# Kernel tuning notes

Hardware: AMD Instinct MI355X
Metric: run time of the kernel (lower is better)

Reference implementation:

```python
import jax, jax.numpy as jnp
import numpy as np


def setup_inputs() -> dict:
    key = jax.random.key(0)
    k1, k2, k3, k4 = jax.random.split(key, 4)
    b, s, h, z = 4, 4096, 2048, 64
    scale = 1.0 / np.sqrt(h)
    return {
        "hidden_states": jax.random.normal(k1, (b, s, h), dtype=jnp.float32),
        # nn.Linear(h, z, bias=False): store as (h, z) so y = x @ W
        "Wq": jax.random.normal(k2, (h, z), dtype=jnp.float32) * scale,
        "Wk": jax.random.normal(k3, (h, z), dtype=jnp.float32) * scale,
        "Wv": jax.random.normal(k4, (h, z), dtype=jnp.float32) * scale,
    }


def reference(hidden_states, Wq, Wk, Wv):
    b, s, h = hidden_states.shape
    z = Wq.shape[1]
    # Three small projections: (b, s, z), cast to float32 as in original
    q = jnp.einsum("bsh,hz->bsz", hidden_states, Wq).astype(jnp.float32)
    k = jnp.einsum("bsh,hz->bsz", hidden_states, Wk).astype(jnp.float32)
    v = jnp.einsum("bsh,hz->bsz", hidden_states, Wv).astype(jnp.float32)
    # Per-token outer product over the expert dim: (b, s, z, z)
    attn = q[..., :, None] * k[..., None, :]
    attn = jax.nn.softmax(attn, axis=-1)
    # Weighted sum over the key expert axis j: out[..., i] = sum_j attn[..., i, j] * v[..., j]
    out = jnp.einsum("bsij,bsj->bsi", attn, v)
    return out.reshape(b * s, z)
```

## Files before the change

kernel.cpp:

```cpp
#include <hip/hip_runtime.h>


typedef __bf16 bf16x8 __attribute__((ext_vector_type(8)));
typedef float f32x4  __attribute__((ext_vector_type(4)));

#define NTOK   16384
#define HDIM   2048
#define NCHUNK 64
#define KCH    32
#define CH_STRIDE (12 * 2 * 512)

#define SWZ(row, kq) ((kq) ^ ((row) & 7))

#define GLOAD_LDS16(g, l)                                                      \
  __builtin_amdgcn_global_load_lds(                                            \
      (const __attribute__((address_space(1))) void*)(g),                      \
      (__attribute__((address_space(3))) void*)(l), 16, 0, 0)

__global__ void pack_w_kernel(const float* __restrict__ Wq,
                              const float* __restrict__ Wk,
                              const float* __restrict__ Wv,
                              __bf16* __restrict__ bfrag)
{
  int u = blockIdx.x * blockDim.x + threadIdx.x;
  if (u >= NCHUNK * 12 * 64) return;
  int l  = u & 63;
  int tn = (u >> 6) % 12;
  int c  = u / (12 * 64);
  int n  = tn * 16 + (l & 15);
  int kb = c * 32 + ((l >> 4) << 3);
  const float* W = (n < 64) ? Wq : (n < 128) ? Wk : Wv;
  int nn = n & 63;
  bf16x8 hi, lo;
#pragma unroll
  for (int j = 0; j < 8; ++j) {
    float f = W[(size_t)(kb + j) * 64 + nn];
    __bf16 h = (__bf16)f;
    hi[j] = h;
    lo[j] = (__bf16)(f - (float)h);
  }
  size_t base = (size_t)(c * 12 + tn) * 1024 + (size_t)l * 8;
  *(bf16x8*)(bfrag + base)       = hi;
  *(bf16x8*)(bfrag + base + 512) = lo;
}

#define LOADB(S, cc)                                                           \
  {                                                                            \
    const __bf16* nbp = bp + (size_t)(cc) * CH_STRIDE;                         \
    _Pragma("unroll")                                                          \
    for (int t = 0; t < 3; ++t) {                                              \
      S##h[t] = *(const bf16x8*)(nbp + (size_t)t * 1024);                      \
      S##l[t] = *(const bf16x8*)(nbp + (size_t)t * 1024 + 512);                \
    }                                                                          \
  }

#define COMPUTE(ab, S)                                                         \
  {                                                                            \
    const int r0 = mr, r1 = 16 + mr;                                           \
    float4 A[4];                                                               \
    A[0] = *(const float4*)&(ab)[r0 * 32 + SWZ(r0, 2 * quad)     * 4];         \
    A[1] = *(const float4*)&(ab)[r0 * 32 + SWZ(r0, 2 * quad + 1) * 4];         \
    A[2] = *(const float4*)&(ab)[r1 * 32 + SWZ(r1, 2 * quad)     * 4];         \
    A[3] = *(const float4*)&(ab)[r1 * 32 + SWZ(r1, 2 * quad + 1) * 4];         \
    bf16x8 ah[2], al[2];                                                       \
    _Pragma("unroll")                                                          \
    for (int i = 0; i < 2; ++i) {                                              \
      float av[8] = {A[2*i].x, A[2*i].y, A[2*i].z, A[2*i].w,                   \
                     A[2*i+1].x, A[2*i+1].y, A[2*i+1].z, A[2*i+1].w};          \
      _Pragma("unroll")                                                        \
      for (int j = 0; j < 8; ++j) {                                            \
        __bf16 h = (__bf16)av[j];                                              \
        ah[i][j] = h;                                                          \
        al[i][j] = (__bf16)(av[j] - (float)h);                                 \
      }                                                                        \
    }                                                                          \
    _Pragma("unroll")                                                          \
    for (int i = 0; i < 2; ++i)                                                \
      _Pragma("unroll")                                                        \
      for (int t = 0; t < 3; ++t) {                                            \
        acc[i][t] = __builtin_amdgcn_mfma_f32_16x16x32_bf16(ah[i], S##h[t], acc[i][t], 0, 0, 0); \
        acc[i][t] = __builtin_amdgcn_mfma_f32_16x16x32_bf16(al[i], S##h[t], acc[i][t], 0, 0, 0); \
        acc[i][t] = __builtin_amdgcn_mfma_f32_16x16x32_bf16(ah[i], S##l[t], acc[i][t], 0, 0, 0); \
      }                                                                        \
  }

__global__ __launch_bounds__(512, 4) void router_kernel(
    const float* __restrict__ x,
    const __bf16* __restrict__ bfrag,
    float* __restrict__ out)
{
  const int tok0 = blockIdx.x * 32;
  const int w    = threadIdx.x >> 6;
  const int lane = threadIdx.x & 63;
  const int kh   = w >> 2;
  const int wc   = w & 3;
  const int mr   = lane & 15;
  const int quad = lane >> 4;

  __shared__ float qkv[2][32 * 196];
  __shared__ float bufA[2][2][1024];

  const int su   = threadIdx.x & 255;
  const int srow = su >> 3;
  const int skq  = su & 7;
  const float* aSrc = x + (size_t)(tok0 + srow) * HDIM + kh * 1024
                        + SWZ(srow, skq) * 4;
  float* aDst0 = &bufA[kh][0][(w & 3) * 256];
  float* aDst1 = &bufA[kh][1][(w & 3) * 256];

  const __bf16* bp = bfrag + (size_t)(kh * KCH) * CH_STRIDE
                           + (size_t)(3 * wc) * 1024 + (size_t)lane * 8;

  f32x4 acc[2][3];
#pragma unroll
  for (int i = 0; i < 2; ++i)
#pragma unroll
    for (int t = 0; t < 3; ++t)
      acc[i][t] = (f32x4){0.f, 0.f, 0.f, 0.f};

  bf16x8 B0h[3], B0l[3], B1h[3], B1l[3];

  GLOAD_LDS16(aSrc, aDst0);
  LOADB(B0, 0)
  __syncthreads();

  for (int c = 0; c < KCH; c += 2) {
    if (c + 1 < KCH) {
      GLOAD_LDS16(aSrc + (c + 1) * 32, aDst1);
      LOADB(B1, c + 1)
    }
    COMPUTE(bufA[kh][0], B0)
    __syncthreads();

    if (c + 2 < KCH) {
      GLOAD_LDS16(aSrc + (c + 2) * 32, aDst0);
      LOADB(B0, c + 2)
    }
    COMPUTE(bufA[kh][1], B1)
    __syncthreads();
  }

#pragma unroll
  for (int i = 0; i < 2; ++i)
#pragma unroll
    for (int t = 0; t < 3; ++t) {
      int col = wc * 48 + t * 16 + mr;
      int row = i * 16 + quad * 4;
#pragma unroll
      for (int r = 0; r < 4; ++r)
        qkv[kh][(row + r) * 196 + col] = acc[i][t][r];
    }
  __syncthreads();

  const int tt = threadIdx.x >> 4;
  const int g  = threadIdx.x & 15;
  const float* q0 = qkv[0] + tt * 196;
  const float* q1 = qkv[1] + tt * 196;
  float qs[4], lsum[4], osum[4];
#pragma unroll
  for (int ii = 0; ii < 4; ++ii) {
    qs[ii]   = (q0[g * 4 + ii] + q1[g * 4 + ii]) * 1.44269504f;
    lsum[ii] = 0.f;
    osum[ii] = 0.f;
  }
  for (int j = 0; j < 64; ++j) {
    float kj = q0[64 + j]  + q1[64 + j];
    float vj = q0[128 + j] + q1[128 + j];
#pragma unroll
    for (int ii = 0; ii < 4; ++ii) {
      float e = __builtin_amdgcn_exp2f(qs[ii] * kj);
      lsum[ii] += e;
      osum[ii] = fmaf(e, vj, osum[ii]);
    }
  }
  float4 r0v;
  r0v.x = osum[0] / lsum[0]; r0v.y = osum[1] / lsum[1];
  r0v.z = osum[2] / lsum[2]; r0v.w = osum[3] / lsum[3];
  float* op = out + (size_t)(tok0 + tt) * 64 + g * 4;
  *(float4*)op = r0v;
}

extern "C" void kernel_launch(void* const* d_in, const int* in_sizes, int n_in,
                              void* d_out, int out_size, void* d_ws, size_t ws_size,
                              hipStream_t stream)
{
  const float* x  = (const float*)d_in[0];
  const float* Wq = (const float*)d_in[1];
  const float* Wk = (const float*)d_in[2];
  const float* Wv = (const float*)d_in[3];
  __bf16* bfrag   = (__bf16*)d_ws;
  float*  out     = (float*)d_out;

  pack_w_kernel<<<(NCHUNK * 12 * 64 + 255) / 256, 256, 0, stream>>>(Wq, Wk, Wv, bfrag);
  router_kernel<<<NTOK / 32, 512, 0, stream>>>(x, bfrag, out);
}
```

Measured before the change: 240.8 us.

## Deepen global-load pipeline with inline-asm B loads and partial vmcnt waits

Replaces the compiler-generated B-fragment loads with inline-asm global_load_dwordx4 using immediate offsets. The main loop is restructured so two chunks of loads (A into LDS and B into registers) stay in flight, using s_waitcnt vmcnt(7) and raw s_barrier in place of full __syncthreads. This aims to overlap memory latency with MFMA compute instead of draining all loads at every barrier. It relies on exact vmcnt counting and sched_barrier placement, so any change in how many loads are issued would silently break correctness.

```diff
diff --git a/kernel.cpp b/kernel.cpp
--- a/kernel.cpp
+++ b/kernel.cpp
@@ -16,6 +16,11 @@
   __builtin_amdgcn_global_load_lds(                                            \
       (const __attribute__((address_space(1))) void*)(g),                      \
       (__attribute__((address_space(3))) void*)(l), 16, 0, 0)
+
+#define WAITV7 asm volatile("s_waitcnt vmcnt(7)" ::: "memory")
+#define WAITV0 asm volatile("s_waitcnt vmcnt(0)" ::: "memory")
+#define SBAR   __builtin_amdgcn_s_barrier()
+#define SCHEDB __builtin_amdgcn_sched_barrier(0)
 
 __global__ void pack_w_kernel(const float* __restrict__ Wq,
                               const float* __restrict__ Wk,
@@ -44,14 +49,22 @@
   *(bf16x8*)(bfrag + base + 512) = lo;
 }
 
-#define LOADB(S, cc)                                                           \
+#define ASMLOADB(S, cc)                                                        \
   {                                                                            \
-    const __bf16* nbp = bp + (size_t)(cc) * CH_STRIDE;                         \
-    _Pragma("unroll")                                                          \
-    for (int t = 0; t < 3; ++t) {                                              \
-      S##h[t] = *(const bf16x8*)(nbp + (size_t)t * 1024);                      \
-      S##l[t] = *(const bf16x8*)(nbp + (size_t)t * 1024 + 512);                \
-    }                                                                          \
+    const __bf16* nbp  = bp + (size_t)(cc) * CH_STRIDE;                        \
+    const __bf16* nbp4 = nbp + 2048;                                           \
+    asm volatile("global_load_dwordx4 %0, %1, off"                             \
+                 : "=&v"(S##h[0]) : "v"(nbp)  : "memory");                     \
+    asm volatile("global_load_dwordx4 %0, %1, off offset:1024"                 \
+                 : "=&v"(S##l[0]) : "v"(nbp)  : "memory");                     \
+    asm volatile("global_load_dwordx4 %0, %1, off offset:2048"                 \
+                 : "=&v"(S##h[1]) : "v"(nbp)  : "memory");                     \
+    asm volatile("global_load_dwordx4 %0, %1, off offset:3072"                 \
+                 : "=&v"(S##l[1]) : "v"(nbp)  : "memory");                     \
+    asm volatile("global_load_dwordx4 %0, %1, off"                             \
+                 : "=&v"(S##h[2]) : "v"(nbp4) : "memory");                     \
+    asm volatile("global_load_dwordx4 %0, %1, off offset:1024"                 \
+                 : "=&v"(S##l[2]) : "v"(nbp4) : "memory");                     \
   }
 
 #define COMPUTE(ab, S)                                                         \
@@ -121,23 +134,29 @@
   bf16x8 B0h[3], B0l[3], B1h[3], B1l[3];
 
   GLOAD_LDS16(aSrc, aDst0);
-  LOADB(B0, 0)
-  __syncthreads();
+  ASMLOADB(B0, 0)
+  GLOAD_LDS16(aSrc + 32, aDst1);
+  ASMLOADB(B1, 1)
 
   for (int c = 0; c < KCH; c += 2) {
-    if (c + 1 < KCH) {
-      GLOAD_LDS16(aSrc + (c + 1) * 32, aDst1);
-      LOADB(B1, c + 1)
-    }
+    WAITV7;
+    SBAR;
+    SCHEDB;
     COMPUTE(bufA[kh][0], B0)
-    __syncthreads();
-
+    SBAR;
     if (c + 2 < KCH) {
       GLOAD_LDS16(aSrc + (c + 2) * 32, aDst0);
-      LOADB(B0, c + 2)
-    }
+      ASMLOADB(B0, c + 2)
+    }
+    if (c + 1 < KCH - 1) { WAITV7; } else { WAITV0; }
+    SBAR;
+    SCHEDB;
     COMPUTE(bufA[kh][1], B1)
-    __syncthreads();
+    SBAR;
+    if (c + 3 < KCH) {
+      GLOAD_LDS16(aSrc + (c + 3) * 32, aDst1);
+      ASMLOADB(B1, c + 3)
+    }
   }
 
 #pragma unroll
```

After: 246.2 us. 2.2% more time.
